# Performance work log

Measured on AMD Instinct MI355X. Metric: run time of the kernel, lower is better.

## Reference

```python
import jax, jax.numpy as jnp
import numpy as np

H, W, A, C = 200, 704, 2, 256   # BEV grid, anchors, feature channels
NC, K = 4, 20000                # peer CAVs, selected anchors per CAV
REG = 7 * A                     # reg head channels


def setup_inputs() -> dict:
    key = jax.random.key(0)
    ks = jax.random.split(key, 8)
    feat = jax.random.normal(ks[0], (1, C, H, W), jnp.float32)
    cls_w = jax.random.normal(ks[1], (A, C), jnp.float32) * 0.02
    cls_b = jnp.zeros((A,), jnp.float32)
    reg_w = jax.random.normal(ks[2], (REG, C), jnp.float32) * 0.02
    reg_b = jnp.zeros((REG,), jnp.float32)
    psm_v2x = jax.random.normal(ks[3], (NC, K), jnp.float32)
    rm_v2x = jax.random.normal(ks[4], (NC, 7 * K), jnp.float32)
    scores_v2x = jax.random.uniform(ks[5], (NC, K), jnp.float32, 0.3, 1.0)
    flat = A * H * W
    idx = []
    for i in range(NC):  # unique sorted flat indices per CAV (masked_select semantics)
        perm = jax.random.permutation(jax.random.fold_in(ks[6], i), flat)[:K]
        idx.append(jnp.sort(perm))
    mask_idx = jnp.stack(idx).astype(jnp.int32)
    # mask_reg = mask.repeat(1,7,1,1): indices tile with offsets r*A*H*W
    offs = (jnp.arange(7) * flat).astype(jnp.int32)
    mask_reg_idx = (mask_idx[:, None, :] + offs[None, :, None]).reshape(NC, 7 * K)
    return {
        'spatial_features_2d': feat, 'cls_w': cls_w, 'cls_b': cls_b,
        'reg_w': reg_w, 'reg_b': reg_b, 'psm_v2x': psm_v2x, 'rm_v2x': rm_v2x,
        'scores_v2x': scores_v2x, 'mask_idx': mask_idx, 'mask_reg_idx': mask_reg_idx,
    }


def _restore(vals, idx, shape):
    # restore_tensor: scatter compacted values into zeros at flat indices, per CAV
    n = vals.shape[0]
    flat = int(np.prod(shape))
    out = jnp.zeros((n, flat), vals.dtype)
    out = out.at[jnp.arange(n)[:, None], idx].set(vals)
    return out.reshape((n,) + shape)


def reference(spatial_features_2d, cls_w, cls_b, reg_w, reg_b,
              psm_v2x, rm_v2x, scores_v2x, mask_idx, mask_reg_idx):
    # 1x1 conv heads
    psm_single = jnp.einsum('bchw,ac->bahw', spatial_features_2d, cls_w) + cls_b[None, :, None, None]
    rm_single = jnp.einsum('bchw,rc->brhw', spatial_features_2d, reg_w) + reg_b[None, :, None, None]
    prob = jax.nn.sigmoid(psm_single)
    # scatter-restore peer CAV results onto the BEV grid
    r_psm = _restore(psm_v2x, mask_idx, (A, H, W))        # [NC,A,H,W]
    r_scores = _restore(scores_v2x, mask_idx, (A, H, W))
    r_rm = _restore(rm_v2x, mask_reg_idx, (REG, H, W))    # [NC,14,H,W]
    psm_all = jnp.concatenate([psm_single, r_psm], axis=0)      # [1+NC,A,H,W]
    prob_all = jnp.concatenate([prob, r_scores], axis=0)
    rm_all = jnp.concatenate([rm_single, r_rm], axis=0)         # [1+NC,14,H,W]
    # per-cell winning CAV by score, then gather psm/rm from the winner
    cav = jnp.argmax(prob_all, axis=0)                    # [A,H,W]
    psm = jnp.take_along_axis(psm_all, cav[None], axis=0) # [1,A,H,W]
    cav_reg = jnp.tile(cav, (7, 1, 1))                    # [14,H,W]
    rm = jnp.take_along_axis(rm_all, cav_reg[None], axis=0)  # [1,14,H,W]
    return psm, rm
```

## Files before the change

kernel.cpp:

```cpp
#include <hip/hip_runtime.h>

#define HH 200
#define WW 704
#define HW (HH * WW)
#define HW4 (HW / 4)
#define AHW (2 * HW)
#define CC 256
#define NCAV 4
#define KK 20000
#define NJ 16

typedef unsigned int u32;

__global__ void scatter_best(const int* __restrict__ mask_idx,
                             const float* __restrict__ scores,
                             u32* __restrict__ winmap) {
    int t = blockIdx.x * blockDim.x + threadIdx.x;
    if (t >= NCAV * KK) return;
    int x = mask_idx[t];
    int n = t / KK;
    union { float f; u32 u; } s;
    s.f = scores[t];
    u32 pack = ((s.u - 0x3E800000u) << 7) | (u32)(3 - n);
    atomicMax(winmap + x, pack);
}

__global__ void prep_weights(const float* __restrict__ cls_w,
                             const float* __restrict__ reg_w,
                             float* __restrict__ wf) {
    int t = blockIdx.x * blockDim.x + threadIdx.x;
    if (t >= NJ * CC) return;
    int c = t >> 4, j = t & 15;
    wf[c * NJ + j] = (j < 2) ? cls_w[j * CC + c] : reg_w[(j - 2) * CC + c];
}

__device__ __forceinline__ int bsearch_row(const int* __restrict__ row, int x) {
    int lo = 0, hi = KK;
    while (lo < hi) {
        int mid = (lo + hi) >> 1;
        if (row[mid] < x) lo = mid + 1; else hi = mid;
    }
    return lo;
}

__global__ __launch_bounds__(128) void head_select(
    const float4* __restrict__ feat4,
    const float* __restrict__ cls_b,
    const float* __restrict__ reg_b,
    const float* __restrict__ psm_v2x,
    const float* __restrict__ rm_v2x,
    const int* __restrict__ mask_idx,
    const float* __restrict__ wf,
    const u32* __restrict__ winmap,
    float* __restrict__ out) {
    int q = blockIdx.x * blockDim.x + threadIdx.x;
    if (q >= HW4) return;
    int pos = q * 4;

    float acc[4][NJ];
#pragma unroll
    for (int j = 0; j < NJ; ++j) {
        float b = (j < 2) ? cls_b[j] : reg_b[j - 2];
        acc[0][j] = b; acc[1][j] = b; acc[2][j] = b; acc[3][j] = b;
    }

#pragma unroll 8
    for (int c = 0; c < CC; ++c) {
        float4 f = feat4[c * HW4 + q];
        const float* wc = wf + c * NJ;
#pragma unroll
        for (int j = 0; j < NJ; ++j) {
            acc[0][j] += f.x * wc[j];
            acc[1][j] += f.y * wc[j];
            acc[2][j] += f.z * wc[j];
            acc[3][j] += f.w * wc[j];
        }
    }

    float4* out4 = (float4*)out;
#pragma unroll
    for (int a = 0; a < 2; ++a) {
        float ps[4], rm[7][4];
#pragma unroll
        for (int e = 0; e < 4; ++e) {
            float p = acc[e][a];
            float prob = 1.0f / (1.0f + expf(-p));
            int x = a * HW + pos + e;
            u32 win = winmap[x];
            float sc = 0.0f;
            if (win != 0u) {
                union { u32 u; float f; } v;
                v.u = (win >> 7) + 0x3E800000u;
                sc = v.f;
            }
            if (sc > prob) {
                int n = 3 - (int)(win & 3u);
                int k = bsearch_row(mask_idx + n * KK, x);
                ps[e] = psm_v2x[n * KK + k];
#pragma unroll
                for (int r = 0; r < 7; ++r)
                    rm[r][e] = rm_v2x[n * (7 * KK) + r * KK + k];
            } else {
                ps[e] = p;
#pragma unroll
                for (int r = 0; r < 7; ++r)
                    rm[r][e] = acc[e][2 + 2 * r + a];
            }
        }
        out4[a * HW4 + q] = make_float4(ps[0], ps[1], ps[2], ps[3]);
#pragma unroll
        for (int r = 0; r < 7; ++r)
            out4[(AHW / 4) + (2 * r + a) * HW4 + q] =
                make_float4(rm[r][0], rm[r][1], rm[r][2], rm[r][3]);
    }
}

extern "C" void kernel_launch(void* const* d_in, const int* in_sizes, int n_in,
                              void* d_out, int out_size, void* d_ws, size_t ws_size,
                              hipStream_t stream) {
    const float* feat    = (const float*)d_in[0];
    const float* cls_w   = (const float*)d_in[1];
    const float* cls_b   = (const float*)d_in[2];
    const float* reg_w   = (const float*)d_in[3];
    const float* reg_b   = (const float*)d_in[4];
    const float* psm_v2x = (const float*)d_in[5];
    const float* rm_v2x  = (const float*)d_in[6];
    const float* scores  = (const float*)d_in[7];
    const int* mask_idx  = (const int*)d_in[8];

    const size_t wf_bytes = (size_t)NJ * CC * sizeof(float);
    const size_t win_bytes = (size_t)AHW * sizeof(u32);
    char* base = (ws_size >= wf_bytes + win_bytes) ? (char*)d_ws : (char*)d_in[9];
    float* wf = (float*)base;
    u32* winmap = (u32*)(base + wf_bytes);

    hipMemsetAsync(winmap, 0, win_bytes, stream);

    scatter_best<<<(NCAV * KK + 255) / 256, 256, 0, stream>>>(mask_idx, scores, winmap);
    prep_weights<<<(NJ * CC + 255) / 256, 256, 0, stream>>>(cls_w, reg_w, wf);
    head_select<<<(HW4 + 127) / 128, 128, 0, stream>>>(
        (const float4*)feat, cls_b, reg_b, psm_v2x, rm_v2x, mask_idx, wf, winmap,
        (float*)d_out);
}
```

Measured before the change: 280.7 us.

## Fuse weight transpose into head kernel and stage weights in LDS

Removes the separate prep_weights kernel launch. Each head_select block now loads and transposes the cls/reg weights into shared memory and reads them as float4 vectors from LDS, where the old code read scalars through global/scalar loads. Block size drops to 64 and the bounds check is removed because HW4 divides evenly by 64. The cost is that every block reloads 16 KB of weights from global memory (the grid is about 550 blocks), and the 16 KB of LDS per block may limit occupancy.

```diff
diff --git a/kernel.cpp b/kernel.cpp
--- a/kernel.cpp
+++ b/kernel.cpp
@@ -25,15 +25,6 @@
     atomicMax(winmap + x, pack);
 }
 
-__global__ void prep_weights(const float* __restrict__ cls_w,
-                             const float* __restrict__ reg_w,
-                             float* __restrict__ wf) {
-    int t = blockIdx.x * blockDim.x + threadIdx.x;
-    if (t >= NJ * CC) return;
-    int c = t >> 4, j = t & 15;
-    wf[c * NJ + j] = (j < 2) ? cls_w[j * CC + c] : reg_w[(j - 2) * CC + c];
-}
-
 __device__ __forceinline__ int bsearch_row(const int* __restrict__ row, int x) {
     int lo = 0, hi = KK;
     while (lo < hi) {
@@ -43,18 +34,27 @@
     return lo;
 }
 
-__global__ __launch_bounds__(128) void head_select(
+__global__ __launch_bounds__(64) void head_select(
     const float4* __restrict__ feat4,
+    const float* __restrict__ cls_w,
+    const float* __restrict__ reg_w,
     const float* __restrict__ cls_b,
     const float* __restrict__ reg_b,
     const float* __restrict__ psm_v2x,
     const float* __restrict__ rm_v2x,
     const int* __restrict__ mask_idx,
-    const float* __restrict__ wf,
     const u32* __restrict__ winmap,
     float* __restrict__ out) {
-    int q = blockIdx.x * blockDim.x + threadIdx.x;
-    if (q >= HW4) return;
+    __shared__ float w_lds[CC * NJ];
+
+    int tid = threadIdx.x;
+    for (int i = tid; i < CC * NJ; i += 64) {
+        int j = i >> 8, c = i & 255;
+        w_lds[c * NJ + j] = (j < 2) ? cls_w[j * CC + c] : reg_w[(j - 2) * CC + c];
+    }
+    __syncthreads();
+
+    int q = blockIdx.x * 64 + tid;
     int pos = q * 4;
 
     float acc[4][NJ];
@@ -67,13 +67,18 @@
 #pragma unroll 8
     for (int c = 0; c < CC; ++c) {
         float4 f = feat4[c * HW4 + q];
-        const float* wc = wf + c * NJ;
+        const float4* wv = (const float4*)&w_lds[c * NJ];
+        float w[NJ];
+        *(float4*)&w[0]  = wv[0];
+        *(float4*)&w[4]  = wv[1];
+        *(float4*)&w[8]  = wv[2];
+        *(float4*)&w[12] = wv[3];
 #pragma unroll
         for (int j = 0; j < NJ; ++j) {
-            acc[0][j] += f.x * wc[j];
-            acc[1][j] += f.y * wc[j];
-            acc[2][j] += f.z * wc[j];
-            acc[3][j] += f.w * wc[j];
+            acc[0][j] += f.x * w[j];
+            acc[1][j] += f.y * w[j];
+            acc[2][j] += f.z * w[j];
+            acc[3][j] += f.w * w[j];
         }
     }
 
@@ -128,17 +133,13 @@
     const float* scores  = (const float*)d_in[7];
     const int* mask_idx  = (const int*)d_in[8];
 
-    const size_t wf_bytes = (size_t)NJ * CC * sizeof(float);
     const size_t win_bytes = (size_t)AHW * sizeof(u32);
-    char* base = (ws_size >= wf_bytes + win_bytes) ? (char*)d_ws : (char*)d_in[9];
-    float* wf = (float*)base;
-    u32* winmap = (u32*)(base + wf_bytes);
+    u32* winmap = (ws_size >= win_bytes) ? (u32*)d_ws : (u32*)d_in[9];
 
     hipMemsetAsync(winmap, 0, win_bytes, stream);
 
     scatter_best<<<(NCAV * KK + 255) / 256, 256, 0, stream>>>(mask_idx, scores, winmap);
-    prep_weights<<<(NJ * CC + 255) / 256, 256, 0, stream>>>(cls_w, reg_w, wf);
-    head_select<<<(HW4 + 127) / 128, 128, 0, stream>>>(
-        (const float4*)feat, cls_b, reg_b, psm_v2x, rm_v2x, mask_idx, wf, winmap,
-        (float*)d_out);
+    head_select<<<HW4 / 64, 64, 0, stream>>>(
+        (const float4*)feat, cls_w, reg_w, cls_b, reg_b,
+        psm_v2x, rm_v2x, mask_idx, winmap, (float*)d_out);
 }
```

After: 298.4 us. 1.06x slower.
